# Optimization experiments

Hardware: AMD Instinct MI355X
Metric: run time of the kernel (lower is better)

Reference implementation:

```python
import jax, jax.numpy as jnp
import numpy as np

NUM_HEADS = 8
LN_EPS = 1e-5


def layer_norm(x, g, b):
    mu = jnp.mean(x, axis=-1, keepdims=True)
    var = jnp.mean(jnp.square(x - mu), axis=-1, keepdims=True)
    return (x - mu) / jnp.sqrt(var + LN_EPS) * g + b


def setup_inputs() -> dict:
    key = jax.random.key(0)
    ks = jax.random.split(key, 16)
    B, N, D, F = 16, 1024, 256, 1024
    s = 0.02
    return {
        "x": jax.random.normal(ks[0], (B, N, D), jnp.float32),
        "spatial_encoding": jax.random.normal(ks[1], (B, N, N), jnp.float32),
        "edge_encoding": jax.random.normal(ks[2], (B, N, N), jnp.float32),
        "gamma1": jnp.ones((D,), jnp.float32),
        "beta1": jnp.zeros((D,), jnp.float32),
        "gamma2": jnp.ones((D,), jnp.float32),
        "beta2": jnp.zeros((D,), jnp.float32),
        "Wq": jax.random.normal(ks[3], (D, D), jnp.float32) * s,
        "Wk": jax.random.normal(ks[4], (D, D), jnp.float32) * s,
        "Wv": jax.random.normal(ks[5], (D, D), jnp.float32) * s,
        "Wo": jax.random.normal(ks[6], (D, D), jnp.float32) * s,
        "W1": jax.random.normal(ks[7], (F, D), jnp.float32) * s,
        "b1": jnp.zeros((F,), jnp.float32),
        "W2": jax.random.normal(ks[8], (D, F), jnp.float32) * s,
        "b2": jnp.zeros((D,), jnp.float32),
    }


def reference(x, spatial_encoding, edge_encoding, gamma1, beta1, gamma2, beta2,
              Wq, Wk, Wv, Wo, W1, b1, W2, b2):
    B, N, D = x.shape
    H = NUM_HEADS
    hd = D // H
    scale = D ** (-0.5)  # source scales by hidden_dim, not head_size

    att_in = layer_norm(x, gamma1, beta1)

    def proj(W):  # [B,N,D] -> [B,H,N,hd]
        return (att_in @ W.T).reshape(B, N, H, hd).transpose(0, 2, 1, 3)

    q, k, v = proj(Wq), proj(Wk), proj(Wv)
    bias = (spatial_encoding + edge_encoding)[:, None]  # [B,1,N,N]
    a = jnp.einsum('bhnd,bhmd->bhnm', q, k) * scale + bias
    pad_mask = jnp.any(a != 0, axis=-1)  # [B,H,N]
    a = jnp.where(pad_mask[..., None], a, -jnp.inf)
    p = jnp.nan_to_num(jax.nn.softmax(a, axis=-1))
    o = jnp.einsum('bhnm,bhmd->bhnd', p, v)
    attn = o.transpose(0, 2, 1, 3).reshape(B, N, D) @ Wo.T
    att_output = attn + x

    pad_mask2 = jnp.any(att_output == 0, axis=-1)  # [B,N]
    ffn_in = layer_norm(x, gamma2, beta2)  # note: norm of x per the source
    h = jax.nn.gelu(ffn_in @ W1.T + b1, approximate=True)
    ffn_out = h @ W2.T + b2 + att_output
    return jnp.where(pad_mask2[..., None], 0.0, ffn_out)
```

## Files before the change

kernel.cpp:

```cpp
#include <hip/hip_runtime.h>
#include <hip/hip_bf16.h>
#include <math.h>

#define Bq 16
#define Nq 1024
#define Dq 256
#define Fq 1024
#define Hq 8
#define HDq 32
#define Mq (Bq * Nq)
#define SCALE 0.0625f
#define LN_EPS 1e-5f

typedef __attribute__((ext_vector_type(8))) short short8;
typedef __attribute__((ext_vector_type(4))) float f32x4;

__device__ __forceinline__ float bf2f(unsigned short s) {
    unsigned u = ((unsigned)s) << 16;
    return __builtin_bit_cast(float, u);
}
__device__ __forceinline__ unsigned short f2bf(float f) {
    __hip_bfloat16 h = __float2bfloat16(f);
    return __builtin_bit_cast(unsigned short, h);
}

typedef __attribute__((address_space(3))) unsigned int lds_uint;
typedef const __attribute__((address_space(1))) unsigned int glb_uint;
__device__ __forceinline__ void async16(void* lds, const void* g) {
    __builtin_amdgcn_global_load_lds((glb_uint*)g, (lds_uint*)lds, 16, 0, 0);
}

__device__ __forceinline__ float gelu_tanh(float v) {
    const float c = 0.7978845608028654f;
    float u = c * (v + 0.044715f * v * v * v);
    return 0.5f * v * (1.0f + tanhf(u));
}

__global__ __launch_bounds__(256) void cvt_weights(
    const float* __restrict__ Wq, const float* __restrict__ Wk,
    const float* __restrict__ Wv, const float* __restrict__ Wo,
    const float* __restrict__ W1, const float* __restrict__ W2,
    unsigned short* __restrict__ dst)
{
    const int blk = blockIdx.x;
    int seg, local;
    if (blk < 256)      { seg = blk >> 6; local = blk & 63; }
    else if (blk < 512) { seg = 4; local = blk - 256; }
    else                { seg = 5; local = blk - 512; }
    const float* srcs[6] = {Wq, Wk, Wv, Wo, W1, W2};
    const size_t dsto[6] = {0, 65536, 131072, 196608, 262144, 524288};
    const float* src = srcs[seg] + (size_t)local * 1024;
    unsigned short* d = dst + dsto[seg] + (size_t)local * 1024;
    const int t4 = threadIdx.x * 4;
    float4 v = *(const float4*)(src + t4);
    uint2 o;
    o.x = (unsigned)f2bf(v.x) | ((unsigned)f2bf(v.y) << 16);
    o.y = (unsigned)f2bf(v.z) | ((unsigned)f2bf(v.w) << 16);
    *(uint2*)(d + t4) = o;
}

__global__ __launch_bounds__(256) void bias_cvt_perm(
    const float* __restrict__ sp, const float* __restrict__ ed,
    unsigned short* __restrict__ P)
{
    const int nt = blockIdx.x, b = blockIdx.y;
    const int t = threadIdx.x;
    __shared__ unsigned short lds[16][1032];
    const size_t src0 = ((size_t)b * Nq + nt * 16) * Nq;

    for (int idx = t; idx < 4096; idx += 256) {
        const int r = idx >> 8, c4 = (idx & 255) * 4;
        float4 a = *(const float4*)(sp + src0 + (size_t)r * Nq + c4);
        float4 e = *(const float4*)(ed + src0 + (size_t)r * Nq + c4);
        uint2 o;
        o.x = (unsigned)f2bf(a.x + e.x) | ((unsigned)f2bf(a.y + e.y) << 16);
        o.y = (unsigned)f2bf(a.z + e.z) | ((unsigned)f2bf(a.w + e.w) << 16);
        *(uint2*)&lds[r][c4] = o;
    }
    __syncthreads();

    unsigned short* Ps = P + ((size_t)(b * 64 + nt) << 14);
    #pragma unroll
    for (int it = 0; it < 8; it++) {
        const int o   = (it * 256 + t) * 8;
        const int r0  = o & 15;
        const int col = (o >> 4) & 15;
        const int mq  = (o >> 8) & 63;
        const int c   = mq * 16 + col;
        uint4 w;
        w.x = (unsigned)lds[r0 + 0][c] | ((unsigned)lds[r0 + 1][c] << 16);
        w.y = (unsigned)lds[r0 + 2][c] | ((unsigned)lds[r0 + 3][c] << 16);
        w.z = (unsigned)lds[r0 + 4][c] | ((unsigned)lds[r0 + 5][c] << 16);
        w.w = (unsigned)lds[r0 + 6][c] | ((unsigned)lds[r0 + 7][c] << 16);
        *(uint4*)(Ps + o) = w;
    }
}

__global__ __launch_bounds__(256) void ln2_kernel(
    const float* __restrict__ x,
    const float* __restrict__ g1, const float* __restrict__ bb1,
    const float* __restrict__ g2, const float* __restrict__ bb2,
    unsigned short* __restrict__ att_in, unsigned short* __restrict__ ffn_in)
{
    const int row = blockIdx.x;
    const int t = threadIdx.x;
    const size_t base = (size_t)row * Dq;
    float v = x[base + t];

    float s = v, sq = v * v;
    #pragma unroll
    for (int off = 32; off > 0; off >>= 1) {
        s  += __shfl_down(s, off);
        sq += __shfl_down(sq, off);
    }
    __shared__ float ssum[4], ssq[4];
    __shared__ float mu_s, rstd_s;
    const int lane = t & 63, wid = t >> 6;
    if (lane == 0) { ssum[wid] = s; ssq[wid] = sq; }
    __syncthreads();
    if (t == 0) {
        float S = ssum[0] + ssum[1] + ssum[2] + ssum[3];
        float Q = ssq[0] + ssq[1] + ssq[2] + ssq[3];
        float mu = S * (1.0f / Dq);
        float var = Q * (1.0f / Dq) - mu * mu;
        mu_s = mu;
        rstd_s = rsqrtf(var + LN_EPS);
    }
    __syncthreads();
    const float nx = (v - mu_s) * rstd_s;
    att_in[base + t] = f2bf(nx * g1[t] + bb1[t]);
    ffn_in[base + t] = f2bf(nx * g2[t] + bb2[t]);
}

#define TM 128
#define TN 128
#define TK 32

__global__ __launch_bounds__(256) void gemm_mfma(
    const unsigned short* __restrict__ A, const unsigned short* __restrict__ W,
    const float* __restrict__ bias, const float* __restrict__ add,
    float* __restrict__ outF, unsigned short* __restrict__ outBF,
    unsigned short* __restrict__ Qb, unsigned short* __restrict__ Kb,
    unsigned short* __restrict__ Vt,
    int M, int Nc, int K, int mode, int apply_gelu)
{
    __shared__ unsigned short As[2][TM * TK];
    __shared__ unsigned short Bs[2][TN * TK];
    const int t = threadIdx.x;
    const int w = t >> 6, lane = t & 63;
    const int col = lane & 15, quad = lane >> 4;
    const int wr = w >> 1, wc = w & 1;
    const int row0 = blockIdx.y * TM;
    const int col0 = blockIdx.x * TN;

    f32x4 acc[4][4] = {};

    const int c0s = w * 128 + lane;
    const int c1s = c0s + 64;
    const int r0s = c0s >> 2, s0s = (c0s & 3) * 8;
    const int r1s = c1s >> 2, s1s = (c1s & 3) * 8;

#define STAGE(buf, kk)                                                        \
    do {                                                                      \
        async16(&As[buf][(w * 128) * 8],      A + (size_t)(row0 + r0s) * K + (kk) + s0s); \
        async16(&Bs[buf][(w * 128) * 8],      W + (size_t)(col0 + r0s) * K + (kk) + s0s); \
        async16(&As[buf][(w * 128 + 64) * 8], A + (size_t)(row0 + r1s) * K + (kk) + s1s); \
        async16(&Bs[buf][(w * 128 + 64) * 8], W + (size_t)(col0 + r1s) * K + (kk) + s1s); \
    } while (0)

    STAGE(0, 0);
    __syncthreads();

    int cur = 0;
    for (int k0 = 0; k0 < K; k0 += TK) {
        if (k0 + TK < K) STAGE(cur ^ 1, k0 + TK);
        short8 wf[4], af[4];
        #pragma unroll
        for (int i = 0; i < 4; i++)
            wf[i] = *(const short8*)&Bs[cur][(wc * 64 + i * 16 + col) * TK + quad * 8];
        #pragma unroll
        for (int j = 0; j < 4; j++)
            af[j] = *(const short8*)&As[cur][(wr * 64 + j * 16 + col) * TK + quad * 8];
        #pragma unroll
        for (int i = 0; i < 4; i++)
            #pragma unroll
            for (int j = 0; j < 4; j++)
                acc[i][j] = __builtin_amdgcn_mfma_f32_16x16x32_bf16(wf[i], af[j], acc[i][j], 0, 0, 0);
        __syncthreads();
        cur ^= 1;
    }
#undef STAGE

    #pragma unroll
    for (int i = 0; i < 4; i++) {
        #pragma unroll
        for (int j = 0; j < 4; j++) {
            const int c0 = col0 + wc * 64 + i * 16 + quad * 4;
            const int r  = row0 + wr * 64 + j * 16 + col;
            float4 v = make_float4(acc[i][j][0], acc[i][j][1], acc[i][j][2], acc[i][j][3]);
            if (mode == 2 && c0 < 256) { v.x *= SCALE; v.y *= SCALE; v.z *= SCALE; v.w *= SCALE; }
            if (bias) {
                float4 bb = *(const float4*)&bias[c0];
                v.x += bb.x; v.y += bb.y; v.z += bb.z; v.w += bb.w;
            }
            if (apply_gelu) {
                v.x = gelu_tanh(v.x); v.y = gelu_tanh(v.y);
                v.z = gelu_tanh(v.z); v.w = gelu_tanh(v.w);
            }
            if (add) {
                float4 aa = *(const float4*)&add[(size_t)r * Nc + c0];
                v.x += aa.x; v.y += aa.y; v.z += aa.z; v.w += aa.w;
            }
            if (mode == 0) {
                *(float4*)&outF[(size_t)r * Nc + c0] = v;
            } else if (mode == 1) {
                uint2 o;
                o.x = (unsigned)f2bf(v.x) | ((unsigned)f2bf(v.y) << 16);
                o.y = (unsigned)f2bf(v.z) | ((unsigned)f2bf(v.w) << 16);
                *(uint2*)&outBF[(size_t)r * Nc + c0] = o;
            } else {
                const int b = r >> 10, n = r & 1023;
                if (c0 < 512) {
                    const int cq = c0 & 255;
                    const int h = cq >> 5, d0 = cq & 31;
                    unsigned short* dst = (c0 < 256 ? Qb : Kb);
                    uint2 o;
                    o.x = (unsigned)f2bf(v.x) | ((unsigned)f2bf(v.y) << 16);
                    o.y = (unsigned)f2bf(v.z) | ((unsigned)f2bf(v.w) << 16);
                    *(uint2*)&dst[(((size_t)(b * Hq + h) << 10) + n) * HDq + d0] = o;
                } else {
                    const int cv = c0 - 512;
                    const int h = cv >> 5, d0 = cv & 31;
                    unsigned short* dst = Vt + (((size_t)(b * Hq + h) * HDq + d0) << 10) + n;
                    dst[0]      = f2bf(v.x);
                    dst[1024]   = f2bf(v.y);
                    dst[2048]   = f2bf(v.z);
                    dst[3072]   = f2bf(v.w);
                }
            }
        }
    }
}

__global__ __launch_bounds__(1024, 4) void attn_mfma(
    const unsigned short* __restrict__ Qbf, const unsigned short* __restrict__ Kbf,
    const unsigned short* __restrict__ Vt, const unsigned short* __restrict__ biasP,
    unsigned short* __restrict__ O16)
{
    const int flat = blockIdx.x;
    const int id2  = (flat & 7) * 32 + (flat >> 3);
    const int b    = id2 >> 4;
    const int h    = (id2 >> 1) & 7;
    const int nh   = id2 & 1;

    const int t = threadIdx.x;
    const int w = t >> 6;
    const int lane = t & 63;
    const int col = lane & 15;
    const int quad = lane >> 4;

    __shared__ unsigned short Klds[32768];
    __shared__ unsigned short Vlds[32768];
    __shared__ unsigned short S16[16][1024];

    const size_t hb = (size_t)b * Hq + h;
    const unsigned short* Qh = Qbf + hb * (Nq * HDq);
    const unsigned short* Kh = Kbf + hb * (Nq * HDq);
    const unsigned short* Vh = Vt  + hb * (HDq * Nq);

    #pragma unroll
    for (int i = 0; i < 4; i++) {
        const int ck = i * 1024 + t;
        async16(&Klds[ck * 8], Kh + ((ck * 8) ^ (((ck >> 3) & 3) << 3)));
        async16(&Vlds[ck * 8], Vh + ((ck * 8) ^ (((ck >> 7) & 7) << 3)));
    }

    const int n0 = nh * 512 + w * 32;
    short8 aq[2];
    #pragma unroll
    for (int qt = 0; qt < 2; qt++)
        aq[qt] = *(const short8*)(Qh + (size_t)(n0 + qt * 16 + col) * HDq + quad * 8);

    const unsigned short* Ps0 = biasP + ((size_t)(b * 64 + nh * 32 + w * 2) << 14);
    unsigned short* Sw = &S16[w][0];

    __syncthreads();

    f32x4 o0[2] = {{0.f,0.f,0.f,0.f},{0.f,0.f,0.f,0.f}};
    f32x4 o1[2] = {{0.f,0.f,0.f,0.f},{0.f,0.f,0.f,0.f}};
    float rsum[2][4] = {};

    for (int tt = 0; tt < 16; tt++) {
        const int k0 = tt * 64;
        short8 kf[4], vf0[2], vf1[2];
        #pragma unroll
        for (int m = 0; m < 4; m++)
            kf[m] = *(const short8*)&Klds[((k0 + m * 16 + col) * 32 + quad * 8)
                                          ^ (((col >> 1) & 3) << 3)];
        #pragma unroll
        for (int c = 0; c < 2; c++) {
            vf0[c] = *(const short8*)&Vlds[((col << 10) + k0 + c * 32 + quad * 8)
                                           ^ ((col & 7) << 3)];
            vf1[c] = *(const short8*)&Vlds[(((col + 16) << 10) + k0 + c * 32 + quad * 8)
                                           ^ ((col & 7) << 3)];
        }
        #pragma unroll
        for (int qt = 0; qt < 2; qt++) {
            const unsigned short* Psq = Ps0 + (qt << 14) + (k0 << 4);
            #pragma unroll
            for (int m = 0; m < 4; m++) {
                f32x4 cc = {0.f, 0.f, 0.f, 0.f};
                cc = __builtin_amdgcn_mfma_f32_16x16x32_bf16(aq[qt], kf[m], cc, 0, 0, 0);
                uint2 bv = *(const uint2*)(Psq + (m << 8) + col * 16 + quad * 4);
                const float bi[4] = {
                    bf2f((unsigned short)(bv.x & 0xffff)), bf2f((unsigned short)(bv.x >> 16)),
                    bf2f((unsigned short)(bv.y & 0xffff)), bf2f((unsigned short)(bv.y >> 16))
                };
                #pragma unroll
                for (int i = 0; i < 4; i++) {
                    const int r = quad * 4 + i;
                    float e = __expf(cc[i] + bi[i]);
                    rsum[qt][i] += e;
                    const int sidx = (r * 64 + m * 16 + col) ^ ((r & 7) << 3);
                    Sw[sidx] = f2bf(e);
                }
            }
            #pragma unroll
            for (int c = 0; c < 2; c++) {
                const int ridx = (col * 64 + c * 32 + quad * 8) ^ ((col & 7) << 3);
                short8 ap = *(const short8*)&Sw[ridx];
                o0[qt] = __builtin_amdgcn_mfma_f32_16x16x32_bf16(ap, vf0[c], o0[qt], 0, 0, 0);
                o1[qt] = __builtin_amdgcn_mfma_f32_16x16x32_bf16(ap, vf1[c], o1[qt], 0, 0, 0);
            }
        }
    }

    #pragma unroll
    for (int qt = 0; qt < 2; qt++) {
        #pragma unroll
        for (int off = 1; off < 16; off <<= 1) {
            #pragma unroll
            for (int i = 0; i < 4; i++) rsum[qt][i] += __shfl_xor(rsum[qt][i], off, 16);
        }
        unsigned short* op = O16 + ((size_t)b * Nq + n0 + qt * 16) * Dq + h * HDq;
        #pragma unroll
        for (int i = 0; i < 4; i++) {
            const float inv = 1.0f / rsum[qt][i];
            const int q = quad * 4 + i;
            op[(size_t)q * Dq + col]      = f2bf(o0[qt][i] * inv);
            op[(size_t)q * Dq + col + 16] = f2bf(o1[qt][i] * inv);
        }
    }
}

__global__ __launch_bounds__(256) void pad2_kernel(
    const float* __restrict__ AO, float* __restrict__ out)
{
    const int row = blockIdx.x;
    const int t = threadIdx.x;
    const float v = AO[(size_t)row * Dq + t];
    unsigned long long m = __ballot(v == 0.0f);
    __shared__ unsigned long long w[4];
    if ((t & 63) == 0) w[t >> 6] = m;
    __syncthreads();
    if ((w[0] | w[1] | w[2] | w[3]) != 0ULL)
        out[(size_t)row * Dq + t] = 0.0f;
}

extern "C" void kernel_launch(void* const* d_in, const int* in_sizes, int n_in,
                              void* d_out, int out_size, void* d_ws, size_t ws_size,
                              hipStream_t stream)
{
    const float* x      = (const float*)d_in[0];
    const float* sp     = (const float*)d_in[1];
    const float* ed     = (const float*)d_in[2];
    const float* gamma1 = (const float*)d_in[3];
    const float* beta1  = (const float*)d_in[4];
    const float* gamma2 = (const float*)d_in[5];
    const float* beta2  = (const float*)d_in[6];
    const float* Wq     = (const float*)d_in[7];
    const float* Wk     = (const float*)d_in[8];
    const float* Wv     = (const float*)d_in[9];
    const float* Wo     = (const float*)d_in[10];
    const float* W1     = (const float*)d_in[11];
    const float* b1     = (const float*)d_in[12];
    const float* W2     = (const float*)d_in[13];
    const float* b2     = (const float*)d_in[14];
    float* out = (float*)d_out;

    unsigned short* s = (unsigned short*)d_ws;
    const size_t MD = (size_t)Mq * Dq;
    unsigned short* att_in16 = s;
    unsigned short* ffn_in16 = s + MD;
    unsigned short* Qbf      = s + 2 * MD;
    unsigned short* Kbf      = s + 3 * MD;
    unsigned short* Vtb      = s + 4 * MD;
    unsigned short* W16      = s + 5 * MD;
    unsigned short* h16      = s + 5 * MD + 786432;
    unsigned short* O16      = att_in16;
    float*          AO       = (float*)Qbf;
    unsigned short* biasP    = h16;

    unsigned short* Wo16 = W16 + 196608;
    unsigned short* W116 = W16 + 262144;
    unsigned short* W216 = W16 + 524288;

    cvt_weights<<<768, 256, 0, stream>>>(Wq, Wk, Wv, Wo, W1, W2, W16);

    bias_cvt_perm<<<dim3(64, 16), 256, 0, stream>>>(sp, ed, biasP);

    ln2_kernel<<<Mq, 256, 0, stream>>>(x, gamma1, beta1, gamma2, beta2, att_in16, ffn_in16);

    dim3 gQKV(768 / TN, Mq / TM);
    gemm_mfma<<<gQKV, 256, 0, stream>>>(att_in16, W16, nullptr, nullptr, nullptr, nullptr,
                                        Qbf, Kbf, Vtb, Mq, 768, Dq, 2, 0);

    attn_mfma<<<256, 1024, 0, stream>>>(Qbf, Kbf, Vtb, biasP, O16);

    dim3 gP(Dq / TN, Mq / TM);
    gemm_mfma<<<gP, 256, 0, stream>>>(O16, Wo16, nullptr, x, AO, nullptr,
                                      nullptr, nullptr, nullptr, Mq, Dq, Dq, 0, 0);

    dim3 gF1(Fq / TN, Mq / TM);
    gemm_mfma<<<gF1, 256, 0, stream>>>(ffn_in16, W116, b1, nullptr, nullptr, h16,
                                       nullptr, nullptr, nullptr, Mq, Fq, Dq, 1, 1);

    gemm_mfma<<<gP, 256, 0, stream>>>(h16, W216, b2, AO, out, nullptr,
                                      nullptr, nullptr, nullptr, Mq, Dq, Fq, 0, 0);

    pad2_kernel<<<Mq, 256, 0, stream>>>(AO, out);
}
```

Measured before the change: 385.8 us.

## Fuse pad mask into GEMM epilogues and drop bias permutation pass

The final pad2 kernel is removed. The Wo projection epilogue now atomically sets a per-row flag when any output element is zero, and the last FFN GEMM zeroes flagged rows before storing. The attention kernel zeroes the flag buffer. The bias is now converted to bf16 in plain row-major order instead of being permuted through LDS. The attention kernel swaps the MFMA operands so each lane holds four contiguous keys of one query, which allows packed 8-byte score stores, a two-shuffle row-sum reduction and row-major bias reads. The intent is to remove one full pass over the activation output and simplify the bias preprocessing. In exchange, bias loads in attention are more strided, and the epilogue adds atomics to the flag buffer.

```diff
diff --git a/kernel.cpp b/kernel.cpp
--- a/kernel.cpp
+++ b/kernel.cpp
@@ -59,41 +59,21 @@
     *(uint2*)(d + t4) = o;
 }
 
-__global__ __launch_bounds__(256) void bias_cvt_perm(
+__global__ __launch_bounds__(256) void bias_cvt(
     const float* __restrict__ sp, const float* __restrict__ ed,
-    unsigned short* __restrict__ P)
-{
-    const int nt = blockIdx.x, b = blockIdx.y;
-    const int t = threadIdx.x;
-    __shared__ unsigned short lds[16][1032];
-    const size_t src0 = ((size_t)b * Nq + nt * 16) * Nq;
-
-    for (int idx = t; idx < 4096; idx += 256) {
-        const int r = idx >> 8, c4 = (idx & 255) * 4;
-        float4 a = *(const float4*)(sp + src0 + (size_t)r * Nq + c4);
-        float4 e = *(const float4*)(ed + src0 + (size_t)r * Nq + c4);
-        uint2 o;
-        o.x = (unsigned)f2bf(a.x + e.x) | ((unsigned)f2bf(a.y + e.y) << 16);
-        o.y = (unsigned)f2bf(a.z + e.z) | ((unsigned)f2bf(a.w + e.w) << 16);
-        *(uint2*)&lds[r][c4] = o;
-    }
-    __syncthreads();
-
-    unsigned short* Ps = P + ((size_t)(b * 64 + nt) << 14);
-    #pragma unroll
-    for (int it = 0; it < 8; it++) {
-        const int o   = (it * 256 + t) * 8;
-        const int r0  = o & 15;
-        const int col = (o >> 4) & 15;
-        const int mq  = (o >> 8) & 63;
-        const int c   = mq * 16 + col;
-        uint4 w;
-        w.x = (unsigned)lds[r0 + 0][c] | ((unsigned)lds[r0 + 1][c] << 16);
-        w.y = (unsigned)lds[r0 + 2][c] | ((unsigned)lds[r0 + 3][c] << 16);
-        w.z = (unsigned)lds[r0 + 4][c] | ((unsigned)lds[r0 + 5][c] << 16);
-        w.w = (unsigned)lds[r0 + 6][c] | ((unsigned)lds[r0 + 7][c] << 16);
-        *(uint4*)(Ps + o) = w;
-    }
+    unsigned short* __restrict__ dst)
+{
+    const size_t i = ((size_t)blockIdx.x * 256 + threadIdx.x) * 8;
+    float4 a0 = *(const float4*)(sp + i);
+    float4 a1 = *(const float4*)(sp + i + 4);
+    float4 e0 = *(const float4*)(ed + i);
+    float4 e1 = *(const float4*)(ed + i + 4);
+    uint4 o;
+    o.x = (unsigned)f2bf(a0.x + e0.x) | ((unsigned)f2bf(a0.y + e0.y) << 16);
+    o.y = (unsigned)f2bf(a0.z + e0.z) | ((unsigned)f2bf(a0.w + e0.w) << 16);
+    o.z = (unsigned)f2bf(a1.x + e1.x) | ((unsigned)f2bf(a1.y + e1.y) << 16);
+    o.w = (unsigned)f2bf(a1.z + e1.z) | ((unsigned)f2bf(a1.w + e1.w) << 16);
+    *(uint4*)(dst + i) = o;
 }
 
 __global__ __launch_bounds__(256) void ln2_kernel(
@@ -142,7 +122,8 @@
     float* __restrict__ outF, unsigned short* __restrict__ outBF,
     unsigned short* __restrict__ Qb, unsigned short* __restrict__ Kb,
     unsigned short* __restrict__ Vt,
-    int M, int Nc, int K, int mode, int apply_gelu)
+    int M, int Nc, int K, int mode, int apply_gelu,
+    unsigned* __restrict__ flagW, const unsigned* __restrict__ flagR)
 {
     __shared__ unsigned short As[2][TM * TK];
     __shared__ unsigned short Bs[2][TN * TK];
@@ -212,6 +193,9 @@
                 v.x += aa.x; v.y += aa.y; v.z += aa.z; v.w += aa.w;
             }
             if (mode == 0) {
+                if (flagR && flagR[r]) { v.x = 0.f; v.y = 0.f; v.z = 0.f; v.w = 0.f; }
+                if (flagW && ((v.x == 0.f) || (v.y == 0.f) || (v.z == 0.f) || (v.w == 0.f)))
+                    atomicOr(&flagW[r], 1u);
                 *(float4*)&outF[(size_t)r * Nc + c0] = v;
             } else if (mode == 1) {
                 uint2 o;
@@ -244,14 +228,16 @@
 
 __global__ __launch_bounds__(1024, 4) void attn_mfma(
     const unsigned short* __restrict__ Qbf, const unsigned short* __restrict__ Kbf,
-    const unsigned short* __restrict__ Vt, const unsigned short* __restrict__ biasP,
-    unsigned short* __restrict__ O16)
+    const unsigned short* __restrict__ Vt, const unsigned short* __restrict__ bias16,
+    unsigned short* __restrict__ O16, unsigned* __restrict__ flags)
 {
     const int flat = blockIdx.x;
-    const int id2  = (flat & 7) * 32 + (flat >> 3);
-    const int b    = id2 >> 4;
-    const int h    = (id2 >> 1) & 7;
-    const int nh   = id2 & 1;
+    const int xg = flat & 7;
+    const int jj = flat >> 3;
+    const int pair = xg * 4 + (jj >> 3);
+    const int b  = pair >> 1;
+    const int nh = pair & 1;
+    const int h  = jj & 7;
 
     const int t = threadIdx.x;
     const int w = t >> 6;
@@ -259,6 +245,8 @@
     const int col = lane & 15;
     const int quad = lane >> 4;
 
+    if (t < 64) flags[flat * 64 + t] = 0;
+
     __shared__ unsigned short Klds[32768];
     __shared__ unsigned short Vlds[32768];
     __shared__ unsigned short S16[16][1024];
@@ -281,14 +269,14 @@
     for (int qt = 0; qt < 2; qt++)
         aq[qt] = *(const short8*)(Qh + (size_t)(n0 + qt * 16 + col) * HDq + quad * 8);
 
-    const unsigned short* Ps0 = biasP + ((size_t)(b * 64 + nh * 32 + w * 2) << 14);
+    const unsigned short* bg = bias16 + ((size_t)b * Nq + n0) * Nq;
     unsigned short* Sw = &S16[w][0];
 
     __syncthreads();
 
     f32x4 o0[2] = {{0.f,0.f,0.f,0.f},{0.f,0.f,0.f,0.f}};
     f32x4 o1[2] = {{0.f,0.f,0.f,0.f},{0.f,0.f,0.f,0.f}};
-    float rsum[2][4] = {};
+    float rsum[2] = {0.f, 0.f};
 
     for (int tt = 0; tt < 16; tt++) {
         const int k0 = tt * 64;
@@ -306,24 +294,22 @@
         }
         #pragma unroll
         for (int qt = 0; qt < 2; qt++) {
-            const unsigned short* Psq = Ps0 + (qt << 14) + (k0 << 4);
+            const unsigned short* bq = bg + (size_t)(qt * 16 + col) * Nq + k0;
             #pragma unroll
             for (int m = 0; m < 4; m++) {
                 f32x4 cc = {0.f, 0.f, 0.f, 0.f};
-                cc = __builtin_amdgcn_mfma_f32_16x16x32_bf16(aq[qt], kf[m], cc, 0, 0, 0);
-                uint2 bv = *(const uint2*)(Psq + (m << 8) + col * 16 + quad * 4);
-                const float bi[4] = {
-                    bf2f((unsigned short)(bv.x & 0xffff)), bf2f((unsigned short)(bv.x >> 16)),
-                    bf2f((unsigned short)(bv.y & 0xffff)), bf2f((unsigned short)(bv.y >> 16))
-                };
-                #pragma unroll
-                for (int i = 0; i < 4; i++) {
-                    const int r = quad * 4 + i;
-                    float e = __expf(cc[i] + bi[i]);
-                    rsum[qt][i] += e;
-                    const int sidx = (r * 64 + m * 16 + col) ^ ((r & 7) << 3);
-                    Sw[sidx] = f2bf(e);
-                }
+                cc = __builtin_amdgcn_mfma_f32_16x16x32_bf16(kf[m], aq[qt], cc, 0, 0, 0);
+                uint2 bv = *(const uint2*)(bq + m * 16 + quad * 4);
+                const float e0 = __expf(cc[0] + bf2f((unsigned short)(bv.x & 0xffff)));
+                const float e1 = __expf(cc[1] + bf2f((unsigned short)(bv.x >> 16)));
+                const float e2 = __expf(cc[2] + bf2f((unsigned short)(bv.y & 0xffff)));
+                const float e3 = __expf(cc[3] + bf2f((unsigned short)(bv.y >> 16)));
+                rsum[qt] += (e0 + e1) + (e2 + e3);
+                uint2 sv;
+                sv.x = (unsigned)f2bf(e0) | ((unsigned)f2bf(e1) << 16);
+                sv.y = (unsigned)f2bf(e2) | ((unsigned)f2bf(e3) << 16);
+                const int widx = (col * 64 + m * 16 + quad * 4) ^ ((col & 7) << 3);
+                *(uint2*)&Sw[widx] = sv;
             }
             #pragma unroll
             for (int c = 0; c < 2; c++) {
@@ -337,34 +323,21 @@
 
     #pragma unroll
     for (int qt = 0; qt < 2; qt++) {
-        #pragma unroll
-        for (int off = 1; off < 16; off <<= 1) {
-            #pragma unroll
-            for (int i = 0; i < 4; i++) rsum[qt][i] += __shfl_xor(rsum[qt][i], off, 16);
-        }
+        rsum[qt] += __shfl_xor(rsum[qt], 16);
+        rsum[qt] += __shfl_xor(rsum[qt], 32);
+    }
+
+    #pragma unroll
+    for (int qt = 0; qt < 2; qt++) {
         unsigned short* op = O16 + ((size_t)b * Nq + n0 + qt * 16) * Dq + h * HDq;
         #pragma unroll
         for (int i = 0; i < 4; i++) {
-            const float inv = 1.0f / rsum[qt][i];
+            const float inv = 1.0f / __shfl(rsum[qt], quad * 4 + i, 16);
             const int q = quad * 4 + i;
             op[(size_t)q * Dq + col]      = f2bf(o0[qt][i] * inv);
             op[(size_t)q * Dq + col + 16] = f2bf(o1[qt][i] * inv);
         }
     }
-}
-
-__global__ __launch_bounds__(256) void pad2_kernel(
-    const float* __restrict__ AO, float* __restrict__ out)
-{
-    const int row = blockIdx.x;
-    const int t = threadIdx.x;
-    const float v = AO[(size_t)row * Dq + t];
-    unsigned long long m = __ballot(v == 0.0f);
-    __shared__ unsigned long long w[4];
-    if ((t & 63) == 0) w[t >> 6] = m;
-    __syncthreads();
-    if ((w[0] | w[1] | w[2] | w[3]) != 0ULL)
-        out[(size_t)row * Dq + t] = 0.0f;
 }
 
 extern "C" void kernel_launch(void* const* d_in, const int* in_sizes, int n_in,
@@ -399,7 +372,8 @@
     unsigned short* h16      = s + 5 * MD + 786432;
     unsigned short* O16      = att_in16;
     float*          AO       = (float*)Qbf;
-    unsigned short* biasP    = h16;
+    unsigned short* bias16   = h16;
+    unsigned*       flags    = (unsigned*)W16;
 
     unsigned short* Wo16 = W16 + 196608;
     unsigned short* W116 = W16 + 262144;
@@ -407,26 +381,27 @@
 
     cvt_weights<<<768, 256, 0, stream>>>(Wq, Wk, Wv, Wo, W1, W2, W16);
 
-    bias_cvt_perm<<<dim3(64, 16), 256, 0, stream>>>(sp, ed, biasP);
+    bias_cvt<<<8192, 256, 0, stream>>>(sp, ed, bias16);
 
     ln2_kernel<<<Mq, 256, 0, stream>>>(x, gamma1, beta1, gamma2, beta2, att_in16, ffn_in16);
 
     dim3 gQKV(768 / TN, Mq / TM);
     gemm_mfma<<<gQKV, 256, 0, stream>>>(att_in16, W16, nullptr, nullptr, nullptr, nullptr,
-                                        Qbf, Kbf, Vtb, Mq, 768, Dq, 2, 0);
-
-    attn_mfma<<<256, 1024, 0, stream>>>(Qbf, Kbf, Vtb, biasP, O16);
+                                        Qbf, Kbf, Vtb, Mq, 768, Dq, 2, 0, nullptr, nullptr);
+
+    attn_mfma<<<256, 1024, 0, stream>>>(Qbf, Kbf, Vtb, bias16, O16, flags);
 
     dim3 gP(Dq / TN, Mq / TM);
     gemm_mfma<<<gP, 256, 0, stream>>>(O16, Wo16, nullptr, x, AO, nullptr,
-                                      nullptr, nullptr, nullptr, Mq, Dq, Dq, 0, 0);
+                                      nullptr, nullptr, nullptr, Mq, Dq, Dq, 0, 0,
+                                      flags, nullptr);
 
     dim3 gF1(Fq / TN, Mq / TM);
     gemm_mfma<<<gF1, 256, 0, stream>>>(ffn_in16, W116, b1, nullptr, nullptr, h16,
-                                       nullptr, nullptr, nullptr, Mq, Fq, Dq, 1, 1);
+                                       nullptr, nullptr, nullptr, Mq, Fq, Dq, 1, 1,
+                                       nullptr, nullptr);
 
     gemm_mfma<<<gP, 256, 0, stream>>>(h16, W216, b2, AO, out, nullptr,
-                                      nullptr, nullptr, nullptr, Mq, Dq, Fq, 0, 0);
-
-    pad2_kernel<<<Mq, 256, 0, stream>>>(AO, out);
-}
+                                      nullptr, nullptr, nullptr, Mq, Dq, Fq, 0, 0,
+                                      nullptr, flags);
+}
```

Measured after the change: 387.5 us. About the same (+0.4%).
